# Performance work log

Hardware: AMD Instinct MI355X
Metric: run time of the kernel (lower is better)

Reference implementation:

```python
import jax, jax.numpy as jnp
import numpy as np

NUM_HEADS = 32
HEAD_DIM = 128
HEAVY_BUDGET = 256
RECENT_BUDGET = 256
ROPE_BASE = 10000.0


def _rope_tables(position_ids, head_dim, dtype):
    inv_freq = 1.0 / (ROPE_BASE ** (jnp.arange(0, head_dim, 2, dtype=jnp.float32) / head_dim))
    freqs = position_ids.astype(jnp.float32)[..., None] * inv_freq  # [b, s, hd/2]
    emb = jnp.concatenate([freqs, freqs], axis=-1)                  # [b, s, hd]
    return jnp.cos(emb).astype(dtype), jnp.sin(emb).astype(dtype)


def _rotate_half(x):
    h = x.shape[-1] // 2
    return jnp.concatenate([-x[..., h:], x[..., :h]], axis=-1)


def setup_inputs() -> dict:
    key = jax.random.key(0)
    k1, k2, k3, k4, k5 = jax.random.split(key, 5)
    b, s, d = 1, 2048, 4096
    hidden_states = jax.random.normal(k1, (b, s, d), dtype=jnp.float32)
    # additive causal mask, as HF passes into forward
    neg = jnp.finfo(jnp.float32).min
    causal = jnp.tril(jnp.ones((s, s), dtype=bool))
    attention_mask = jnp.where(causal, 0.0, neg).astype(jnp.float32)[None, None]  # [1,1,s,s]
    position_ids = jnp.arange(s, dtype=jnp.int32)[None]  # [1, s]
    scale = 0.02
    Wq = jax.random.normal(k2, (d, d), dtype=jnp.float32) * scale
    Wk = jax.random.normal(k3, (d, d), dtype=jnp.float32) * scale
    Wv = jax.random.normal(k4, (d, d), dtype=jnp.float32) * scale
    Wo = jax.random.normal(k5, (d, d), dtype=jnp.float32) * scale
    return {"hidden_states": hidden_states, "attention_mask": attention_mask,
            "position_ids": position_ids, "Wq": Wq, "Wk": Wk, "Wv": Wv, "Wo": Wo}


def reference(hidden_states, attention_mask, position_ids, Wq, Wk, Wv, Wo):
    b, s, d = hidden_states.shape
    H, hd = NUM_HEADS, HEAD_DIM
    kv = s  # prefill: no past_key_value, masks reset

    # projections: nn.Linear(x) = x @ W.T
    q = (hidden_states @ Wq.T).reshape(b, s, H, hd).transpose(0, 2, 1, 3)  # [b,H,s,hd]
    k = (hidden_states @ Wk.T).reshape(b, s, H, hd).transpose(0, 2, 1, 3)
    v = (hidden_states @ Wv.T).reshape(b, s, H, hd).transpose(0, 2, 1, 3)

    cos, sin = _rope_tables(position_ids, hd, q.dtype)  # [b,s,hd]
    cos, sin = cos[:, None], sin[:, None]               # broadcast over heads
    q = q * cos + _rotate_half(q) * sin
    k = k * cos + _rotate_half(k) * sin

    attn = jnp.einsum('bhqd,bhkd->bhqk', q, k) / np.float32(np.sqrt(hd))
    neg = jnp.finfo(attn.dtype).min
    attn = jnp.maximum(attn + attention_mask, neg)
    # attention_masks_next is None on the first (prefill) call -> no multiplicative mask here
    attn = jax.nn.softmax(attn.astype(jnp.float32), axis=-1).astype(q.dtype)  # [b,H,s,kv]

    # running per-head score accumulation: sum over batch and query dims
    scores = attn.sum(axis=0).sum(axis=1)  # [H, kv]; previous_scores is None at prefill

    # heavy-hitter eviction mask for the next decode step (kv+1 columns)
    mask = jnp.ones((H, kv + 1), dtype=attn.dtype)
    # attn_tokens_all (=kv) > cache_budget, recent_budget > 0:
    mask = mask.at[:, :kv + 1 - RECENT_BUDGET].set(0.0)
    selected = scores[:, :kv - RECENT_BUDGET]                    # drop recent region
    _, keep_topk = jax.lax.top_k(selected, HEAVY_BUDGET)         # [H, heavy]
    mask = mask.at[jnp.arange(H)[:, None], keep_topk].set(1.0)   # scatter heavy hitters
    # torch aliasing: score_mask = attn_mask[:, :-1]; score_mask[:, -recent:] = 1 mutates attn_mask too
    mask = mask.at[:, kv - RECENT_BUDGET:kv].set(1.0)
    attention_masks_next = mask[None, :, None, :]                # [1,H,1,kv+1]
    previous_scores = scores * mask[:, :kv]                      # masked score state

    out = jnp.einsum('bhqk,bhkd->bhqd', attn, v)                 # [b,H,s,hd]
    out = out.transpose(0, 2, 1, 3).reshape(b, s, d) @ Wo.T
    return out, attention_masks_next, previous_scores
```

## Files before the change

### kernel.cpp

```cpp
#include <hip/hip_runtime.h>
#include <hip/hip_bf16.h>
#include <cmath>

#define S_LEN 2048
#define DMODEL 4096
#define NH 32
#define HDIM 128
#define HEAVY 256
#define RECENT 256
#define ATTN_SCALE 0.08838834764831845f
#define NEGBIG -3.0e38f
#define MB (1024ull * 1024ull)

typedef __attribute__((ext_vector_type(8))) short short8v;
typedef __attribute__((ext_vector_type(4))) short short4v;
typedef __attribute__((ext_vector_type(4))) float floatx4;

__device__ inline ushort f2bf(float x) {
  __hip_bfloat16 h = __float2bfloat16(x);
  return __builtin_bit_cast(ushort, h);
}
struct Split3 {
  short a, b, c;
};
__device__ inline Split3 split3(float x) {
  unsigned u = __float_as_uint(x);
  unsigned u1 = u & 0xFFFF0000u;
  float r1 = x - __uint_as_float(u1);
  unsigned u2 = __float_as_uint(r1) & 0xFFFF0000u;
  float r2 = r1 - __uint_as_float(u2);
  unsigned u3 = __float_as_uint(r2);
  Split3 o;
  o.a = (short)(u1 >> 16);
  o.b = (short)(u2 >> 16);
  o.c = (short)(u3 >> 16);
  return o;
}

__device__ __forceinline__ void gl_lds16(const short* gsrc, short* ldst) {
  __builtin_amdgcn_global_load_lds((const __attribute__((address_space(1))) void*)gsrc,
                                   (__attribute__((address_space(3))) void*)ldst, 16, 0, 0);
}

__global__ void split_mat(const float* __restrict__ X, short* __restrict__ Xa,
                          short* __restrict__ Xb, short* __restrict__ Xc, int n4) {
  int stride = gridDim.x * blockDim.x;
  for (int i = blockIdx.x * blockDim.x + threadIdx.x; i < n4; i += stride) {
    float4 v = reinterpret_cast<const float4*>(X)[i];
    float vv[4] = {v.x, v.y, v.z, v.w};
    short4v a, b, c;
#pragma unroll
    for (int j = 0; j < 4; j++) {
      Split3 t = split3(vv[j]);
      a[j] = t.a; b[j] = t.b; c[j] = t.c;
    }
    reinterpret_cast<short4v*>(Xa)[i] = a;
    reinterpret_cast<short4v*>(Xb)[i] = b;
    reinterpret_cast<short4v*>(Xc)[i] = c;
  }
}

__global__ __launch_bounds__(256) void norms_kernel(const float* __restrict__ Qf,
                                                    const float* __restrict__ Kf,
                                                    float* __restrict__ qn,
                                                    float* __restrict__ mk2p) {
  const int h = blockIdx.x >> 4, ch = blockIdx.x & 15;
  const int wv = threadIdx.x >> 6, lane = threadIdx.x & 63;
  __shared__ float wmax[4];
  float mx = 0.f;
  for (int i = 0; i < 32; i++) {
    int r = ch * 128 + wv * 32 + i;
    const float2 qv =
        *reinterpret_cast<const float2*>(&Qf[(size_t)r * DMODEL + h * HDIM + lane * 2]);
    const float2 kv =
        *reinterpret_cast<const float2*>(&Kf[(size_t)r * DMODEL + h * HDIM + lane * 2]);
    float sq = qv.x * qv.x + qv.y * qv.y;
    float sk = kv.x * kv.x + kv.y * kv.y;
#pragma unroll
    for (int off = 1; off <= 32; off <<= 1) {
      sq += __shfl_xor(sq, off);
      sk += __shfl_xor(sk, off);
    }
    if (lane == 0) qn[h * S_LEN + r] = sqrtf(sq);
    mx = fmaxf(mx, sk);
  }
  if (lane == 0) wmax[wv] = mx;
  __syncthreads();
  if (threadIdx.x == 0)
    mk2p[blockIdx.x] = fmaxf(fmaxf(wmax[0], wmax[1]), fmaxf(wmax[2], wmax[3]));
}

__global__ __launch_bounds__(256, 3) void gemm6p(
    const short* __restrict__ Aag, const short* __restrict__ Abg, const short* __restrict__ Acg,
    const short* __restrict__ Bag, const short* __restrict__ Bbg, const short* __restrict__ Bcg,
    float* __restrict__ C, int M, int N, int K) {
  __shared__ short LP[6][128 * 32];
  const int tid = threadIdx.x;
  const int w = tid >> 6, l = tid & 63, g = l >> 4, ln = l & 15;
  const int wm = w >> 1, wn = w & 1;
  const int row0 = blockIdx.y * 128, col0 = blockIdx.x * 128;
  const int wb = tid & 192;
  floatx4 acc[4][4] = {};
  for (int k0 = 0; k0 < K; k0 += 32) {
    __syncthreads();
#pragma unroll
    for (int it = 0; it < 2; it++) {
      int id = it * 256 + tid;
      int r = id >> 2, j = id & 3;
      int cg = j ^ ((r >> 1) & 3);
      size_t ga = (size_t)(row0 + r) * K + k0 + cg * 8;
      size_t gb = (size_t)(col0 + r) * K + k0 + cg * 8;
      int cb = (it * 256 + wb) * 8;
      gl_lds16(Aag + ga, &LP[0][cb]);
      gl_lds16(Abg + ga, &LP[1][cb]);
      gl_lds16(Acg + ga, &LP[2][cb]);
      gl_lds16(Bag + gb, &LP[3][cb]);
      gl_lds16(Bbg + gb, &LP[4][cb]);
      gl_lds16(Bcg + gb, &LP[5][cb]);
    }
    __syncthreads();
#pragma unroll
    for (int i = 0; i < 4; i++) {
      int arow = wm * 64 + i * 16 + ln;
      int aoff = arow * 32 + ((g ^ ((arow >> 1) & 3)) * 8);
      short8v a1 = *reinterpret_cast<const short8v*>(&LP[0][aoff]);
      short8v a2 = *reinterpret_cast<const short8v*>(&LP[1][aoff]);
      short8v a3 = *reinterpret_cast<const short8v*>(&LP[2][aoff]);
#pragma unroll
      for (int j = 0; j < 4; j++) {
        int brow = wn * 64 + j * 16 + ln;
        int boff = brow * 32 + ((g ^ ((brow >> 1) & 3)) * 8);
        short8v b1 = *reinterpret_cast<const short8v*>(&LP[3][boff]);
        short8v b2 = *reinterpret_cast<const short8v*>(&LP[4][boff]);
        short8v b3 = *reinterpret_cast<const short8v*>(&LP[5][boff]);
        acc[i][j] = __builtin_amdgcn_mfma_f32_16x16x32_bf16(a1, b1, acc[i][j], 0, 0, 0);
        acc[i][j] = __builtin_amdgcn_mfma_f32_16x16x32_bf16(a1, b2, acc[i][j], 0, 0, 0);
        acc[i][j] = __builtin_amdgcn_mfma_f32_16x16x32_bf16(a2, b1, acc[i][j], 0, 0, 0);
        acc[i][j] = __builtin_amdgcn_mfma_f32_16x16x32_bf16(a1, b3, acc[i][j], 0, 0, 0);
        acc[i][j] = __builtin_amdgcn_mfma_f32_16x16x32_bf16(a2, b2, acc[i][j], 0, 0, 0);
        acc[i][j] = __builtin_amdgcn_mfma_f32_16x16x32_bf16(a3, b1, acc[i][j], 0, 0, 0);
      }
    }
  }
#pragma unroll
  for (int i = 0; i < 4; i++)
#pragma unroll
    for (int j = 0; j < 4; j++)
#pragma unroll
      for (int r = 0; r < 4; r++)
        C[(size_t)(row0 + wm * 64 + i * 16 + g * 4 + r) * N + col0 + wn * 64 + j * 16 + ln] =
            acc[i][j][r];
}

__global__ __launch_bounds__(256) void gemm6h(const short* __restrict__ Aag,
                                              const short* __restrict__ Abg,
                                              const short* __restrict__ Acg,
                                              const float* __restrict__ B,
                                              float* __restrict__ C, int M, int N, int K) {
  __shared__ short Aa[128 * 40], Ab[128 * 40], Ac[128 * 40];
  __shared__ short Ba[128 * 40], Bb[128 * 40], Bc[128 * 40];
  const int tid = threadIdx.x;
  const int w = tid >> 6, l = tid & 63, g = l >> 4, ln = l & 15;
  const int wm = w >> 1, wn = w & 1;
  const int row0 = blockIdx.y * 128, col0 = blockIdx.x * 128;
  floatx4 acc[4][4] = {};
  for (int k0 = 0; k0 < K; k0 += 32) {
    __syncthreads();
#pragma unroll
    for (int i = 0; i < 2; i++) {
      int id = tid + i * 256;
      int r = id >> 2, c = id & 3;
      size_t ga = (size_t)(row0 + r) * K + k0 + c * 8;
      int o = r * 40 + c * 8;
      *reinterpret_cast<short8v*>(&Aa[o]) = *reinterpret_cast<const short8v*>(&Aag[ga]);
      *reinterpret_cast<short8v*>(&Ab[o]) = *reinterpret_cast<const short8v*>(&Abg[ga]);
      *reinterpret_cast<short8v*>(&Ac[o]) = *reinterpret_cast<const short8v*>(&Acg[ga]);
    }
#pragma unroll
    for (int i = 0; i < 4; i++) {
      int id = tid + i * 256;
      int r = id >> 3, c4 = id & 7;
      float4 bv = *reinterpret_cast<const float4*>(&B[(size_t)(col0 + r) * K + k0 + c4 * 4]);
      float bf[4] = {bv.x, bv.y, bv.z, bv.w};
      short4v b1, b2, b3;
#pragma unroll
      for (int j = 0; j < 4; j++) {
        Split3 t = split3(bf[j]);
        b1[j] = t.a; b2[j] = t.b; b3[j] = t.c;
      }
      int o = r * 40 + c4 * 4;
      *reinterpret_cast<short4v*>(&Ba[o]) = b1;
      *reinterpret_cast<short4v*>(&Bb[o]) = b2;
      *reinterpret_cast<short4v*>(&Bc[o]) = b3;
    }
    __syncthreads();
#pragma unroll
    for (int i = 0; i < 4; i++) {
      int ar = (wm * 64 + i * 16 + ln) * 40 + g * 8;
      short8v a1 = *reinterpret_cast<const short8v*>(&Aa[ar]);
      short8v a2 = *reinterpret_cast<const short8v*>(&Ab[ar]);
      short8v a3 = *reinterpret_cast<const short8v*>(&Ac[ar]);
#pragma unroll
      for (int j = 0; j < 4; j++) {
        int br = (wn * 64 + j * 16 + ln) * 40 + g * 8;
        short8v b1 = *reinterpret_cast<const short8v*>(&Ba[br]);
        short8v b2 = *reinterpret_cast<const short8v*>(&Bb[br]);
        short8v b3 = *reinterpret_cast<const short8v*>(&Bc[br]);
        acc[i][j] = __builtin_amdgcn_mfma_f32_16x16x32_bf16(a1, b1, acc[i][j], 0, 0, 0);
        acc[i][j] = __builtin_amdgcn_mfma_f32_16x16x32_bf16(a1, b2, acc[i][j], 0, 0, 0);
        acc[i][j] = __builtin_amdgcn_mfma_f32_16x16x32_bf16(a2, b1, acc[i][j], 0, 0, 0);
        acc[i][j] = __builtin_amdgcn_mfma_f32_16x16x32_bf16(a1, b3, acc[i][j], 0, 0, 0);
        acc[i][j] = __builtin_amdgcn_mfma_f32_16x16x32_bf16(a2, b2, acc[i][j], 0, 0, 0);
        acc[i][j] = __builtin_amdgcn_mfma_f32_16x16x32_bf16(a3, b1, acc[i][j], 0, 0, 0);
      }
    }
  }
#pragma unroll
  for (int i = 0; i < 4; i++)
#pragma unroll
    for (int j = 0; j < 4; j++)
#pragma unroll
      for (int r = 0; r < 4; r++)
        C[(size_t)(row0 + wm * 64 + i * 16 + g * 4 + r) * N + col0 + wn * 64 + j * 16 + ln] =
            acc[i][j][r];
}

__global__ __launch_bounds__(256) void gemm_bf1(const float* __restrict__ A,
                                                const float* __restrict__ B,
                                                float* __restrict__ C, int M, int N, int K) {
  __shared__ short Ah[128 * 56];
  __shared__ short Bh[128 * 56];
  const int tid = threadIdx.x;
  const int w = tid >> 6, l = tid & 63, g = l >> 4, ln = l & 15;
  const int wm = w >> 1, wn = w & 1;
  const int row0 = blockIdx.y * 128, col0 = blockIdx.x * 128;
  floatx4 acc[4][4] = {};
  for (int k0 = 0; k0 < K; k0 += 32) {
    __syncthreads();
#pragma unroll
    for (int i = 0; i < 4; i++) {
      int id = tid + i * 256;
      int r = id >> 3, c4 = id & 7;
      float4 av = *reinterpret_cast<const float4*>(&A[(size_t)(row0 + r) * K + k0 + c4 * 4]);
      float4 bv = *reinterpret_cast<const float4*>(&B[(size_t)(col0 + r) * K + k0 + c4 * 4]);
      short4v ah, bh;
      ah[0] = (short)f2bf(av.x); ah[1] = (short)f2bf(av.y);
      ah[2] = (short)f2bf(av.z); ah[3] = (short)f2bf(av.w);
      bh[0] = (short)f2bf(bv.x); bh[1] = (short)f2bf(bv.y);
      bh[2] = (short)f2bf(bv.z); bh[3] = (short)f2bf(bv.w);
      *reinterpret_cast<short4v*>(&Ah[r * 56 + c4 * 4]) = ah;
      *reinterpret_cast<short4v*>(&Bh[r * 56 + c4 * 4]) = bh;
    }
    __syncthreads();
#pragma unroll
    for (int i = 0; i < 4; i++) {
      short8v a = *reinterpret_cast<const short8v*>(&Ah[(wm * 64 + i * 16 + ln) * 56 + g * 8]);
#pragma unroll
      for (int j = 0; j < 4; j++) {
        short8v b = *reinterpret_cast<const short8v*>(&Bh[(wn * 64 + j * 16 + ln) * 56 + g * 8]);
        acc[i][j] = __builtin_amdgcn_mfma_f32_16x16x32_bf16(a, b, acc[i][j], 0, 0, 0);
      }
    }
  }
#pragma unroll
  for (int i = 0; i < 4; i++)
#pragma unroll
    for (int j = 0; j < 4; j++)
#pragma unroll
      for (int r = 0; r < 4; r++)
        C[(size_t)(row0 + wm * 64 + i * 16 + g * 4 + r) * N + col0 + wn * 64 + j * 16 + ln] =
            acc[i][j][r];
}

__global__ __launch_bounds__(256) void gemm_vbt(const short* __restrict__ Ab2,
                                                const float* __restrict__ B,
                                                ushort* __restrict__ Vt, int M, int N, int K) {
  __shared__ short Ah[128 * 56];
  __shared__ short Bh[128 * 56];
  const int tid = threadIdx.x;
  const int w = tid >> 6, l = tid & 63, g = l >> 4, ln = l & 15;
  const int wm = w >> 1, wn = w & 1;
  const int row0 = blockIdx.y * 128, col0 = blockIdx.x * 128;
  floatx4 acc[4][4] = {};
  for (int k0 = 0; k0 < K; k0 += 32) {
    __syncthreads();
#pragma unroll
    for (int i = 0; i < 2; i++) {
      int id = tid + i * 256;
      int r = id >> 2, c = id & 3;
      *reinterpret_cast<short8v*>(&Ah[r * 56 + c * 8]) =
          *reinterpret_cast<const short8v*>(&Ab2[(size_t)(row0 + r) * K + k0 + c * 8]);
    }
#pragma unroll
    for (int i = 0; i < 4; i++) {
      int id = tid + i * 256;
      int r = id >> 3, c4 = id & 7;
      float4 bv = *reinterpret_cast<const float4*>(&B[(size_t)(col0 + r) * K + k0 + c4 * 4]);
      short4v bh;
      bh[0] = (short)f2bf(bv.x); bh[1] = (short)f2bf(bv.y);
      bh[2] = (short)f2bf(bv.z); bh[3] = (short)f2bf(bv.w);
      *reinterpret_cast<short4v*>(&Bh[r * 56 + c4 * 4]) = bh;
    }
    __syncthreads();
#pragma unroll
    for (int i = 0; i < 4; i++) {
      short8v a = *reinterpret_cast<const short8v*>(&Ah[(wm * 64 + i * 16 + ln) * 56 + g * 8]);
#pragma unroll
      for (int j = 0; j < 4; j++) {
        short8v b = *reinterpret_cast<const short8v*>(&Bh[(wn * 64 + j * 16 + ln) * 56 + g * 8]);
        acc[i][j] = __builtin_amdgcn_mfma_f32_16x16x32_bf16(a, b, acc[i][j], 0, 0, 0);
      }
    }
  }
#pragma unroll
  for (int i = 0; i < 4; i++)
#pragma unroll
    for (int j = 0; j < 4; j++) {
      short4v o;
#pragma unroll
      for (int r = 0; r < 4; r++) o[r] = (short)f2bf(acc[i][j][r]);
      size_t n = col0 + wn * 64 + j * 16 + ln;
      size_t m0 = row0 + wm * 64 + i * 16 + g * 4;
      *reinterpret_cast<short4v*>(&Vt[n * M + m0]) = o;
    }
}

__global__ void rope_convert(const float* __restrict__ Q, const float* __restrict__ K,
                             const int* __restrict__ pos, short* __restrict__ Qa,
                             short* __restrict__ Qb, short* __restrict__ Qc,
                             short* __restrict__ Ka, short* __restrict__ Kb,
                             short* __restrict__ Kc) {
  int idx = blockIdx.x * blockDim.x + threadIdx.x;
  if (idx >= S_LEN * 64) return;
  int d = idx & 63;
  int r = idx >> 6;
  float p = (float)pos[r];
  float invf = (float)pow(10000.0, -(double)(2 * d) / 128.0);
  float ang = p * invf;
  float c = cosf(ang), s = sinf(ang);
  for (int h = 0; h < NH; h++) {
    size_t base = (size_t)r * DMODEL + h * HDIM + d;
    float q1 = Q[base], q2 = Q[base + 64];
    float k1 = K[base], k2 = K[base + 64];
    float qa = q1 * c - q2 * s, qb = q2 * c + q1 * s;
    float ka = k1 * c - k2 * s, kb = k2 * c + k1 * s;
    Split3 t;
    t = split3(qa); Qa[base] = t.a; Qb[base] = t.b; Qc[base] = t.c;
    t = split3(qb); Qa[base + 64] = t.a; Qb[base + 64] = t.b; Qc[base + 64] = t.c;
    t = split3(ka); Ka[base] = t.a; Kb[base] = t.b; Kc[base] = t.c;
    t = split3(kb); Ka[base + 64] = t.a; Kb[base + 64] = t.b; Kc[base + 64] = t.c;
  }
}

#define KVB 32
#define KSPL (KVB * 128)

__device__ __forceinline__ floatx4 qk6_tile(const short* KaS, const short* KbS,
                                            const short* KcS, const short8v q1[4],
                                            const short8v q2[4], const short8v q3[4],
                                            int krow, int g) {
  floatx4 cA = {}, cB = {}, cC = {}, cD = {}, cE = {}, cF = {};
#pragma unroll
  for (int dc = 0; dc < 4; dc++) {
    int didx = krow * 128 + ((dc * 32 + g * 8) ^ ((krow & 7) << 3));
    short8v k1 = *reinterpret_cast<const short8v*>(&KaS[didx]);
    short8v k2 = *reinterpret_cast<const short8v*>(&KbS[didx]);
    short8v k3 = *reinterpret_cast<const short8v*>(&KcS[didx]);
    cA = __builtin_amdgcn_mfma_f32_16x16x32_bf16(q1[dc], k1, cA, 0, 0, 0);
    cB = __builtin_amdgcn_mfma_f32_16x16x32_bf16(q1[dc], k2, cB, 0, 0, 0);
    cC = __builtin_amdgcn_mfma_f32_16x16x32_bf16(q2[dc], k1, cC, 0, 0, 0);
    cD = __builtin_amdgcn_mfma_f32_16x16x32_bf16(q1[dc], k3, cD, 0, 0, 0);
    cE = __builtin_amdgcn_mfma_f32_16x16x32_bf16(q2[dc], k2, cE, 0, 0, 0);
    cF = __builtin_amdgcn_mfma_f32_16x16x32_bf16(q3[dc], k1, cF, 0, 0, 0);
  }
  return ((cA + cB) + (cC + cD)) + (cE + cF);
}

__device__ __forceinline__ void issue_tile(const short* __restrict__ Ka,
                                           const short* __restrict__ Kb,
                                           const short* __restrict__ Kc, int k0, int h,
                                           short* bufA, short* bufB, short* bufC, int tid) {
  const int wb = tid & 192;
#pragma unroll
  for (int it = 0; it < 2; it++) {
    int j = it * 256 + tid;
    int r = j >> 4, cl = j & 15;
    int cg = cl ^ (r & 7);
    size_t goff = (size_t)(k0 + r) * DMODEL + h * HDIM + cg * 8;
    int cb = (it * 256 + wb) * 8;
    gl_lds16(Ka + goff, bufA + cb);
    gl_lds16(Kb + goff, bufB + cb);
    gl_lds16(Kc + goff, bufC + cb);
  }
}

__global__ __launch_bounds__(256, 3) void attn_fused(
    const short* __restrict__ Qa, const short* __restrict__ Qb, const short* __restrict__ Qc,
    const short* __restrict__ Ka, const short* __restrict__ Kb, const short* __restrict__ Kc,
    const ushort* __restrict__ Vt, const float* __restrict__ qn,
    const float* __restrict__ mk2p, float* __restrict__ AO, float* __restrict__ sp4) {
  __shared__ short KS[2][3][KSPL];
  __shared__ short Ps[4 * 512];
  const int bid = blockIdx.x;
  const int qb = 31 - (bid >> 5);
  const int h = bid & 31;
  const int tid = threadIdx.x;
  const int w = tid >> 6, g = (tid >> 4) & 3, ln = tid & 15;
  const int q0 = qb * 64;
  const int qrow = q0 + w * 16 + ln;
  short8v q1[4], q2[4], q3[4];
#pragma unroll
  for (int dc = 0; dc < 4; dc++) {
    size_t off = (size_t)qrow * DMODEL + h * HDIM + dc * 32 + g * 8;
    q1[dc] = *reinterpret_cast<const short8v*>(&Qa[off]);
    q2[dc] = *reinterpret_cast<const short8v*>(&Qb[off]);
    q3[dc] = *reinterpret_cast<const short8v*>(&Qc[off]);
  }
  float mkv = 0.f;
#pragma unroll
  for (int j = 0; j < 16; j++) mkv = fmaxf(mkv, mk2p[h * 16 + j]);
  const float mk = sqrtf(mkv);
  float B_r[4], l_r[4];
#pragma unroll
  for (int r = 0; r < 4; r++) {
    B_r[r] = qn[h * S_LEN + q0 + w * 16 + g * 4 + r] * mk * ATTN_SCALE;
    l_r[r] = 0.f;
  }
  const int nkt = 2 * qb + 2;

  issue_tile(Ka, Kb, Kc, 0, h, KS[0][0], KS[0][1], KS[0][2], tid);
  __syncthreads();
  for (int t = 0; t < nkt; t++) {
    const int k0 = t * KVB;
    const int cur = t & 1;
    if (t + 1 < nkt)
      issue_tile(Ka, Kb, Kc, k0 + KVB, h, KS[cur ^ 1][0], KS[cur ^ 1][1], KS[cur ^ 1][2], tid);
#pragma unroll
    for (int ct = 0; ct < 2; ct++) {
      floatx4 sacc = qk6_tile(KS[cur][0], KS[cur][1], KS[cur][2], q1, q2, q3, ct * 16 + ln, g);
#pragma unroll
      for (int r = 0; r < 4; r++) {
        float s = sacc[r] * ATTN_SCALE;
        int key = k0 + ct * 16 + ln;
        int qq = q0 + w * 16 + g * 4 + r;
        l_r[r] += (key <= qq) ? __expf(s - B_r[r]) : 0.f;
      }
    }
    __syncthreads();
  }
  float inv_l[4];
#pragma unroll
  for (int r = 0; r < 4; r++) {
    float l = l_r[r];
    l += __shfl_xor(l, 1);
    l += __shfl_xor(l, 2);
    l += __shfl_xor(l, 4);
    l += __shfl_xor(l, 8);
    inv_l[r] = 1.0f / l;
  }

  floatx4 o[8] = {};
  issue_tile(Ka, Kb, Kc, 0, h, KS[0][0], KS[0][1], KS[0][2], tid);
  __syncthreads();
  for (int t = 0; t < nkt; t++) {
    const int k0 = t * KVB;
    const int cur = t & 1;
    if (t + 1 < nkt)
      issue_tile(Ka, Kb, Kc, k0 + KVB, h, KS[cur ^ 1][0], KS[cur ^ 1][1], KS[cur ^ 1][2], tid);
    float pv[2][4];
#pragma unroll
    for (int ct = 0; ct < 2; ct++) {
      floatx4 sacc = qk6_tile(KS[cur][0], KS[cur][1], KS[cur][2], q1, q2, q3, ct * 16 + ln, g);
#pragma unroll
      for (int r = 0; r < 4; r++) {
        float s = sacc[r] * ATTN_SCALE;
        int key = k0 + ct * 16 + ln;
        int qq = q0 + w * 16 + g * 4 + r;
        float e = (key <= qq) ? __expf(s - B_r[r]) : 0.f;
        pv[ct][r] = e * inv_l[r];
      }
    }
#pragma unroll
    for (int ct = 0; ct < 2; ct++) {
      float c2 = pv[ct][0] + pv[ct][1] + pv[ct][2] + pv[ct][3];
      c2 += __shfl_xor(c2, 16);
      c2 += __shfl_xor(c2, 32);
      if (g == 0) sp4[((size_t)(qb * 4 + w) * NH + h) * S_LEN + k0 + ct * 16 + ln] = c2;
    }
#pragma unroll
    for (int ct = 0; ct < 2; ct++)
#pragma unroll
      for (int r = 0; r < 4; r++) {
        int prow = g * 4 + r, pcol = ct * 16 + ln;
        Ps[w * 512 + prow * 32 + (pcol ^ (((prow >> 1) & 1) << 4))] = (short)f2bf(pv[ct][r]);
      }
    short8v pa = *reinterpret_cast<const short8v*>(
        &Ps[w * 512 + ln * 32 + ((g * 8) ^ (((ln >> 1) & 1) << 4))]);
#pragma unroll
    for (int ctd = 0; ctd < 8; ctd++) {
      size_t voff = ((size_t)h * HDIM + ctd * 16 + ln) * S_LEN + k0 + g * 8;
      short8v vb = *reinterpret_cast<const short8v*>(&Vt[voff]);
      o[ctd] = __builtin_amdgcn_mfma_f32_16x16x32_bf16(pa, vb, o[ctd], 0, 0, 0);
    }
    __syncthreads();
  }
#pragma unroll
  for (int ctd = 0; ctd < 8; ctd++)
#pragma unroll
    for (int r = 0; r < 4; r++)
      AO[(size_t)(q0 + w * 16 + g * 4 + r) * DMODEL + h * HDIM + ctd * 16 + ln] = o[ctd][r];
}

__global__ void reduce_scores(const float* __restrict__ sp4, float* __restrict__ scores) {
  int idx = blockIdx.x * blockDim.x + threadIdx.x;
  if (idx >= NH * S_LEN) return;
  int h = idx >> 11, k = idx & 2047;
  float s = 0.f;
  for (int j = 0; j < 128; j++) s += sp4[((size_t)j * NH + h) * S_LEN + k];
  scores[idx] = s;
}

__global__ __launch_bounds__(256) void topk_mask_kernel(const float* __restrict__ scores,
                                                        float* __restrict__ out_mask,
                                                        float* __restrict__ prev_scores) {
  const int h = blockIdx.x;
  __shared__ unsigned sb[S_LEN - RECENT];
  __shared__ int cnt_sh;
  const int NSEL = S_LEN - RECENT;
  const int tid = threadIdx.x;
  const float* sc = scores + (size_t)h * S_LEN;
  for (int i = tid; i < NSEL; i += 256) sb[i] = __float_as_uint(sc[i]);
  __syncthreads();
  unsigned prefix = 0u;
  for (int b = 31; b >= 0; b--) {
    unsigned cand = prefix | (1u << b);
    if (tid == 0) cnt_sh = 0;
    __syncthreads();
    int c = 0;
    for (int i = tid; i < NSEL; i += 256) c += (sb[i] >= cand) ? 1 : 0;
    atomicAdd(&cnt_sh, c);
    __syncthreads();
    if (cnt_sh >= HEAVY) prefix = cand;
    __syncthreads();
  }
  if (tid == 0) cnt_sh = 0;
  __syncthreads();
  int c = 0;
  for (int i = tid; i < NSEL; i += 256) c += (sb[i] > prefix) ? 1 : 0;
  atomicAdd(&cnt_sh, c);
  __syncthreads();
  const int c1 = cnt_sh;
  float* mrow = out_mask + (size_t)h * (S_LEN + 1);
  float* prow = prev_scores + (size_t)h * S_LEN;
  for (int j = NSEL + tid; j < S_LEN + 1; j += 256) mrow[j] = 1.0f;
  for (int k = NSEL + tid; k < S_LEN; k += 256) prow[k] = sc[k];
  for (int i = tid; i < NSEL; i += 256) {
    bool sel = sb[i] > prefix;
    mrow[i] = sel ? 1.f : 0.f;
    prow[i] = sel ? sc[i] : 0.f;
  }
  __syncthreads();
  if (tid == 0) {
    int need = HEAVY - c1;
    for (int i = 0; i < NSEL && need > 0; i++) {
      if (sb[i] == prefix) { mrow[i] = 1.f; prow[i] = sc[i]; need--; }
    }
  }
}

extern "C" void kernel_launch(void* const* d_in, const int* in_sizes, int n_in,
                              void* d_out, int out_size, void* d_ws, size_t ws_size,
                              hipStream_t stream) {
  const float* hidden = (const float*)d_in[0];
  const int* pos = (const int*)d_in[2];
  const float* Wq = (const float*)d_in[3];
  const float* Wk = (const float*)d_in[4];
  const float* Wv = (const float*)d_in[5];
  const float* Wo = (const float*)d_in[6];

  float* out0 = (float*)d_out;
  float* out_mask = out0 + (size_t)S_LEN * DMODEL;
  float* prev_scores = out_mask + (size_t)NH * (S_LEN + 1);

  char* ws = (char*)d_ws;
  float* Qf = (float*)(ws + 0 * MB);
  float* Kf = (float*)(ws + 32 * MB);
  ushort* Vt = (ushort*)(ws + 64 * MB);
  short* Ha = (short*)(ws + 80 * MB);
  short* Hb = (short*)(ws + 96 * MB);
  short* Hc = (short*)(ws + 112 * MB);
  short* Qa = (short*)(ws + 80 * MB);
  short* Qb = (short*)(ws + 96 * MB);
  short* Qc = (short*)(ws + 112 * MB);
  short* Ka = (short*)(ws + 128 * MB);
  short* Kb = (short*)(ws + 144 * MB);
  short* Kc = (short*)(ws + 160 * MB);
  float* AO = Qf;
  float* sp4 = Kf;
  float* scores = (float*)(ws + 64 * MB);

  float* qn = out0;
  float* mk2p = out0 + NH * S_LEN;

  dim3 gg(DMODEL / 128, S_LEN / 128);
  split_mat<<<2048, 256, 0, stream>>>(hidden, Ha, Hb, Hc, S_LEN * DMODEL / 4);

  if (ws_size >= 224 * MB) {
    short* Wsa = (short*)(ws + 128 * MB);
    short* Wsb = (short*)(ws + 160 * MB);
    short* Wsc = (short*)(ws + 192 * MB);
    split_mat<<<2048, 256, 0, stream>>>(Wq, Wsa, Wsb, Wsc, DMODEL * DMODEL / 4);
    gemm6p<<<gg, 256, 0, stream>>>(Ha, Hb, Hc, Wsa, Wsb, Wsc, Qf, S_LEN, DMODEL, DMODEL);
    split_mat<<<2048, 256, 0, stream>>>(Wk, Wsa, Wsb, Wsc, DMODEL * DMODEL / 4);
    gemm6p<<<gg, 256, 0, stream>>>(Ha, Hb, Hc, Wsa, Wsb, Wsc, Kf, S_LEN, DMODEL, DMODEL);
  } else {
    gemm6h<<<gg, 256, 0, stream>>>(Ha, Hb, Hc, Wq, Qf, S_LEN, DMODEL, DMODEL);
    gemm6h<<<gg, 256, 0, stream>>>(Ha, Hb, Hc, Wk, Kf, S_LEN, DMODEL, DMODEL);
  }
  gemm_vbt<<<gg, 256, 0, stream>>>(Ha, Wv, Vt, S_LEN, DMODEL, DMODEL);

  norms_kernel<<<512, 256, 0, stream>>>(Qf, Kf, qn, mk2p);

  int rope_total = S_LEN * 64;
  rope_convert<<<(rope_total + 255) / 256, 256, 0, stream>>>(Qf, Kf, pos, Qa, Qb, Qc, Ka, Kb, Kc);

  hipError_t _e = hipMemsetAsync(sp4, 0, (size_t)128 * NH * S_LEN * sizeof(float), stream);
  (void)_e;
  attn_fused<<<1024, 256, 0, stream>>>(Qa, Qb, Qc, Ka, Kb, Kc, Vt, qn, mk2p, AO, sp4);

  reduce_scores<<<(NH * S_LEN + 255) / 256, 256, 0, stream>>>(sp4, scores);
  topk_mask_kernel<<<NH, 256, 0, stream>>>(scores, out_mask, prev_scores);

  gemm_bf1<<<gg, 256, 0, stream>>>(AO, Wo, out0, S_LEN, DMODEL, DMODEL);
}
```

Measured before the change: 1.610 ms.

## Pre-convert Wv/Wo to bf16 and use double-buffered async-LDS bf16 GEMM

Adds a to_bf16 conversion kernel and replaces the V and output projections with a templated bf16×bf16 GEMM. It double-buffers direct global-to-LDS loads with an XOR swizzle, and sets launch bounds to 3 blocks per CU. The attention kernel now writes its output as bf16, and its P-tile LDS swizzle is changed to reduce bank conflicts. This removes the per-tile fp32-to-bf16 conversion inside the GEMM mainloops and halves the bytes loaded, at the cost of two extra weight conversion passes and extra workspace traffic.

```diff
diff --git a/kernel.cpp b/kernel.cpp
--- a/kernel.cpp
+++ b/kernel.cpp
@@ -57,6 +57,19 @@
     reinterpret_cast<short4v*>(Xa)[i] = a;
     reinterpret_cast<short4v*>(Xb)[i] = b;
     reinterpret_cast<short4v*>(Xc)[i] = c;
+  }
+}
+
+__global__ void to_bf16(const float* __restrict__ X, ushort* __restrict__ Y, int n4) {
+  int stride = gridDim.x * blockDim.x;
+  for (int i = blockIdx.x * blockDim.x + threadIdx.x; i < n4; i += stride) {
+    float4 v = reinterpret_cast<const float4*>(X)[i];
+    short4v o;
+    o[0] = (short)f2bf(v.x);
+    o[1] = (short)f2bf(v.y);
+    o[2] = (short)f2bf(v.z);
+    o[3] = (short)f2bf(v.w);
+    reinterpret_cast<short4v*>(Y)[i] = o;
   }
 }
 
@@ -225,104 +238,78 @@
             acc[i][j][r];
 }
 
-__global__ __launch_bounds__(256) void gemm_bf1(const float* __restrict__ A,
-                                                const float* __restrict__ B,
-                                                float* __restrict__ C, int M, int N, int K) {
-  __shared__ short Ah[128 * 56];
-  __shared__ short Bh[128 * 56];
+template <int TOUT>
+__global__ __launch_bounds__(256, 3) void gemm_bb(const short* __restrict__ A,
+                                                  const short* __restrict__ B, void* Cv, int M,
+                                                  int N, int K) {
+  __shared__ short KS[2][2][128 * 32];
   const int tid = threadIdx.x;
   const int w = tid >> 6, l = tid & 63, g = l >> 4, ln = l & 15;
   const int wm = w >> 1, wn = w & 1;
   const int row0 = blockIdx.y * 128, col0 = blockIdx.x * 128;
+  const int wb = tid & 192;
   floatx4 acc[4][4] = {};
-  for (int k0 = 0; k0 < K; k0 += 32) {
-    __syncthreads();
+  const int nt = K / 32;
+  auto issue = [&](int k0, int buf) {
+#pragma unroll
+    for (int it = 0; it < 2; it++) {
+      int id = it * 256 + tid;
+      int r = id >> 2, j = id & 3;
+      int cg = j ^ ((r >> 1) & 3);
+      size_t ga = (size_t)(row0 + r) * K + k0 + cg * 8;
+      size_t gb = (size_t)(col0 + r) * K + k0 + cg * 8;
+      int cb = (it * 256 + wb) * 8;
+      gl_lds16(A + ga, &KS[buf][0][cb]);
+      gl_lds16(B + gb, &KS[buf][1][cb]);
+    }
+  };
+  issue(0, 0);
+  __syncthreads();
+  for (int t = 0; t < nt; t++) {
+    const int cur = t & 1;
+    if (t + 1 < nt) issue((t + 1) * 32, cur ^ 1);
+    short8v b[4];
+#pragma unroll
+    for (int j = 0; j < 4; j++) {
+      int brow = wn * 64 + j * 16 + ln;
+      b[j] = *reinterpret_cast<const short8v*>(
+          &KS[cur][1][brow * 32 + ((g ^ ((brow >> 1) & 3)) * 8)]);
+    }
 #pragma unroll
     for (int i = 0; i < 4; i++) {
-      int id = tid + i * 256;
-      int r = id >> 3, c4 = id & 7;
-      float4 av = *reinterpret_cast<const float4*>(&A[(size_t)(row0 + r) * K + k0 + c4 * 4]);
-      float4 bv = *reinterpret_cast<const float4*>(&B[(size_t)(col0 + r) * K + k0 + c4 * 4]);
-      short4v ah, bh;
-      ah[0] = (short)f2bf(av.x); ah[1] = (short)f2bf(av.y);
-      ah[2] = (short)f2bf(av.z); ah[3] = (short)f2bf(av.w);
-      bh[0] = (short)f2bf(bv.x); bh[1] = (short)f2bf(bv.y);
-      bh[2] = (short)f2bf(bv.z); bh[3] = (short)f2bf(bv.w);
-      *reinterpret_cast<short4v*>(&Ah[r * 56 + c4 * 4]) = ah;
-      *reinterpret_cast<short4v*>(&Bh[r * 56 + c4 * 4]) = bh;
-    }
-    __syncthreads();
-#pragma unroll
-    for (int i = 0; i < 4; i++) {
-      short8v a = *reinterpret_cast<const short8v*>(&Ah[(wm * 64 + i * 16 + ln) * 56 + g * 8]);
+      int arow = wm * 64 + i * 16 + ln;
+      short8v a = *reinterpret_cast<const short8v*>(
+          &KS[cur][0][arow * 32 + ((g ^ ((arow >> 1) & 3)) * 8)]);
+#pragma unroll
+      for (int j = 0; j < 4; j++)
+        acc[i][j] = __builtin_amdgcn_mfma_f32_16x16x32_bf16(a, b[j], acc[i][j], 0, 0, 0);
+    }
+    __syncthreads();
+  }
+  if (TOUT == 0) {
+    float* C = (float*)Cv;
+#pragma unroll
+    for (int i = 0; i < 4; i++)
+#pragma unroll
+      for (int j = 0; j < 4; j++)
+#pragma unroll
+        for (int r = 0; r < 4; r++)
+          C[(size_t)(row0 + wm * 64 + i * 16 + g * 4 + r) * N + col0 + wn * 64 + j * 16 + ln] =
+              acc[i][j][r];
+  } else {
+    ushort* Vt = (ushort*)Cv;
+#pragma unroll
+    for (int i = 0; i < 4; i++)
 #pragma unroll
       for (int j = 0; j < 4; j++) {
-        short8v b = *reinterpret_cast<const short8v*>(&Bh[(wn * 64 + j * 16 + ln) * 56 + g * 8]);
-        acc[i][j] = __builtin_amdgcn_mfma_f32_16x16x32_bf16(a, b, acc[i][j], 0, 0, 0);
+        short4v o;
+#pragma unroll
+        for (int r = 0; r < 4; r++) o[r] = (short)f2bf(acc[i][j][r]);
+        size_t n = col0 + wn * 64 + j * 16 + ln;
+        size_t m0 = row0 + wm * 64 + i * 16 + g * 4;
+        *reinterpret_cast<short4v*>(&Vt[n * M + m0]) = o;
       }
-    }
-  }
-#pragma unroll
-  for (int i = 0; i < 4; i++)
-#pragma unroll
-    for (int j = 0; j < 4; j++)
-#pragma unroll
-      for (int r = 0; r < 4; r++)
-        C[(size_t)(row0 + wm * 64 + i * 16 + g * 4 + r) * N + col0 + wn * 64 + j * 16 + ln] =
-            acc[i][j][r];
-}
-
-__global__ __launch_bounds__(256) void gemm_vbt(const short* __restrict__ Ab2,
-                                                const float* __restrict__ B,
-                                                ushort* __restrict__ Vt, int M, int N, int K) {
-  __shared__ short Ah[128 * 56];
-  __shared__ short Bh[128 * 56];
-  const int tid = threadIdx.x;
-  const int w = tid >> 6, l = tid & 63, g = l >> 4, ln = l & 15;
-  const int wm = w >> 1, wn = w & 1;
-  const int row0 = blockIdx.y * 128, col0 = blockIdx.x * 128;
-  floatx4 acc[4][4] = {};
-  for (int k0 = 0; k0 < K; k0 += 32) {
-    __syncthreads();
-#pragma unroll
-    for (int i = 0; i < 2; i++) {
-      int id = tid + i * 256;
-      int r = id >> 2, c = id & 3;
-      *reinterpret_cast<short8v*>(&Ah[r * 56 + c * 8]) =
-          *reinterpret_cast<const short8v*>(&Ab2[(size_t)(row0 + r) * K + k0 + c * 8]);
-    }
-#pragma unroll
-    for (int i = 0; i < 4; i++) {
-      int id = tid + i * 256;
-      int r = id >> 3, c4 = id & 7;
-      float4 bv = *reinterpret_cast<const float4*>(&B[(size_t)(col0 + r) * K + k0 + c4 * 4]);
-      short4v bh;
-      bh[0] = (short)f2bf(bv.x); bh[1] = (short)f2bf(bv.y);
-      bh[2] = (short)f2bf(bv.z); bh[3] = (short)f2bf(bv.w);
-      *reinterpret_cast<short4v*>(&Bh[r * 56 + c4 * 4]) = bh;
-    }
-    __syncthreads();
-#pragma unroll
-    for (int i = 0; i < 4; i++) {
-      short8v a = *reinterpret_cast<const short8v*>(&Ah[(wm * 64 + i * 16 + ln) * 56 + g * 8]);
-#pragma unroll
-      for (int j = 0; j < 4; j++) {
-        short8v b = *reinterpret_cast<const short8v*>(&Bh[(wn * 64 + j * 16 + ln) * 56 + g * 8]);
-        acc[i][j] = __builtin_amdgcn_mfma_f32_16x16x32_bf16(a, b, acc[i][j], 0, 0, 0);
-      }
-    }
-  }
-#pragma unroll
-  for (int i = 0; i < 4; i++)
-#pragma unroll
-    for (int j = 0; j < 4; j++) {
-      short4v o;
-#pragma unroll
-      for (int r = 0; r < 4; r++) o[r] = (short)f2bf(acc[i][j][r]);
-      size_t n = col0 + wn * 64 + j * 16 + ln;
-      size_t m0 = row0 + wm * 64 + i * 16 + g * 4;
-      *reinterpret_cast<short4v*>(&Vt[n * M + m0]) = o;
-    }
+  }
 }
 
 __global__ void rope_convert(const float* __restrict__ Q, const float* __restrict__ K,
@@ -398,7 +385,7 @@
     const short* __restrict__ Qa, const short* __restrict__ Qb, const short* __restrict__ Qc,
     const short* __restrict__ Ka, const short* __restrict__ Kb, const short* __restrict__ Kc,
     const ushort* __restrict__ Vt, const float* __restrict__ qn,
-    const float* __restrict__ mk2p, float* __restrict__ AO, float* __restrict__ sp4) {
+    const float* __restrict__ mk2p, ushort* __restrict__ AObf, float* __restrict__ sp4) {
   __shared__ short KS[2][3][KSPL];
   __shared__ short Ps[4 * 512];
   const int bid = blockIdx.x;
@@ -492,10 +479,11 @@
 #pragma unroll
       for (int r = 0; r < 4; r++) {
         int prow = g * 4 + r, pcol = ct * 16 + ln;
-        Ps[w * 512 + prow * 32 + (pcol ^ (((prow >> 1) & 1) << 4))] = (short)f2bf(pv[ct][r]);
+        int col = ((((pcol >> 3) ^ (prow >> 2)) & 3) << 3) | (pcol & 7);
+        Ps[w * 512 + prow * 32 + col] = (short)f2bf(pv[ct][r]);
       }
     short8v pa = *reinterpret_cast<const short8v*>(
-        &Ps[w * 512 + ln * 32 + ((g * 8) ^ (((ln >> 1) & 1) << 4))]);
+        &Ps[w * 512 + ln * 32 + (((g ^ (ln >> 2)) & 3) << 3)]);
 #pragma unroll
     for (int ctd = 0; ctd < 8; ctd++) {
       size_t voff = ((size_t)h * HDIM + ctd * 16 + ln) * S_LEN + k0 + g * 8;
@@ -508,7 +496,8 @@
   for (int ctd = 0; ctd < 8; ctd++)
 #pragma unroll
     for (int r = 0; r < 4; r++)
-      AO[(size_t)(q0 + w * 16 + g * 4 + r) * DMODEL + h * HDIM + ctd * 16 + ln] = o[ctd][r];
+      AObf[(size_t)(q0 + w * 16 + g * 4 + r) * DMODEL + h * HDIM + ctd * 16 + ln] =
+          f2bf(o[ctd][r]);
 }
 
 __global__ void reduce_scores(const float* __restrict__ sp4, float* __restrict__ scores) {
@@ -595,9 +584,10 @@
   short* Ka = (short*)(ws + 128 * MB);
   short* Kb = (short*)(ws + 144 * MB);
   short* Kc = (short*)(ws + 160 * MB);
-  float* AO = Qf;
+  ushort* AObf = (ushort*)(ws + 0 * MB);
   float* sp4 = Kf;
   float* scores = (float*)(ws + 64 * MB);
+  ushort* Wobf = (ushort*)(ws + 96 * MB);
 
   float* qn = out0;
   float* mk2p = out0 + NH * S_LEN;
@@ -605,6 +595,7 @@
   dim3 gg(DMODEL / 128, S_LEN / 128);
   split_mat<<<2048, 256, 0, stream>>>(hidden, Ha, Hb, Hc, S_LEN * DMODEL / 4);
 
+  ushort* Wvbf;
   if (ws_size >= 224 * MB) {
     short* Wsa = (short*)(ws + 128 * MB);
     short* Wsb = (short*)(ws + 160 * MB);
@@ -613,11 +604,14 @@
     gemm6p<<<gg, 256, 0, stream>>>(Ha, Hb, Hc, Wsa, Wsb, Wsc, Qf, S_LEN, DMODEL, DMODEL);
     split_mat<<<2048, 256, 0, stream>>>(Wk, Wsa, Wsb, Wsc, DMODEL * DMODEL / 4);
     gemm6p<<<gg, 256, 0, stream>>>(Ha, Hb, Hc, Wsa, Wsb, Wsc, Kf, S_LEN, DMODEL, DMODEL);
+    Wvbf = (ushort*)(ws + 192 * MB);
   } else {
     gemm6h<<<gg, 256, 0, stream>>>(Ha, Hb, Hc, Wq, Qf, S_LEN, DMODEL, DMODEL);
     gemm6h<<<gg, 256, 0, stream>>>(Ha, Hb, Hc, Wk, Kf, S_LEN, DMODEL, DMODEL);
-  }
-  gemm_vbt<<<gg, 256, 0, stream>>>(Ha, Wv, Vt, S_LEN, DMODEL, DMODEL);
+    Wvbf = (ushort*)(ws + 128 * MB);
+  }
+  to_bf16<<<2048, 256, 0, stream>>>(Wv, Wvbf, DMODEL * DMODEL / 4);
+  gemm_bb<1><<<gg, 256, 0, stream>>>(Ha, (const short*)Wvbf, Vt, S_LEN, DMODEL, DMODEL);
 
   norms_kernel<<<512, 256, 0, stream>>>(Qf, Kf, qn, mk2p);
 
@@ -626,10 +620,12 @@
 
   hipError_t _e = hipMemsetAsync(sp4, 0, (size_t)128 * NH * S_LEN * sizeof(float), stream);
   (void)_e;
-  attn_fused<<<1024, 256, 0, stream>>>(Qa, Qb, Qc, Ka, Kb, Kc, Vt, qn, mk2p, AO, sp4);
-
+  attn_fused<<<1024, 256, 0, stream>>>(Qa, Qb, Qc, Ka, Kb, Kc, Vt, qn, mk2p, AObf, sp4);
+
+  to_bf16<<<2048, 256, 0, stream>>>(Wo, Wobf, DMODEL * DMODEL / 4);
   reduce_scores<<<(NH * S_LEN + 255) / 256, 256, 0, stream>>>(sp4, scores);
   topk_mask_kernel<<<NH, 256, 0, stream>>>(scores, out_mask, prev_scores);
 
-  gemm_bf1<<<gg, 256, 0, stream>>>(AO, Wo, out0, S_LEN, DMODEL, DMODEL);
-}
+  gemm_bb<0><<<gg, 256, 0, stream>>>((const short*)AObf, (const short*)Wobf, out0, S_LEN, DMODEL,
+                                     DMODEL);
+}
```

Result: faster. 1.466 ms (-8.9%).
